# Kernel tuning notes

Hardware: AMD Instinct MI355X
Metric: run time of the kernel (lower is better)

## Reference

```python
import jax, jax.numpy as jnp
import numpy as np

B, S, D = 8, 3840, 384
G, H, E = 30, 48, 8          # groups, heads, head_dim (D == H*E)
SL = S // G                   # local window length = 128


def setup_inputs() -> dict:
    key = jax.random.key(0)
    ks = jax.random.split(key, 6)
    std = 0.05  # matches nn.init.normal_(std=0.05)
    return {
        "inputs": jax.random.normal(ks[0], (B, S, D), jnp.float32),
        "conquer": jax.random.normal(ks[1], (B, 1, D), jnp.float32),
        "mask_local": jnp.zeros((B, G, SL, SL), jnp.bool_),
        "mask_conquer": jnp.zeros((B, G, SL), jnp.bool_),
        "W_Query": jax.random.normal(ks[2], (D, D), jnp.float32) * std,
        "W_Key": jax.random.normal(ks[3], (D, D), jnp.float32) * std,
        "W_Value": jax.random.normal(ks[4], (D, D), jnp.float32) * std,
        "ln_gamma": jnp.ones((D,), jnp.float32),
        "ln_beta": jnp.zeros((D,), jnp.float32),
    }


def _layer_norm(x, gamma, beta, eps=1e-5):
    mu = jnp.mean(x, axis=-1, keepdims=True)
    var = jnp.mean(jnp.square(x - mu), axis=-1, keepdims=True)
    return (x - mu) * jax.lax.rsqrt(var + eps) * gamma + beta


def reference(inputs, conquer, mask_local, mask_conquer, W_Query, W_Key, W_Value, ln_gamma, ln_beta):
    b, s, d = inputs.shape
    N = b * G  # number of (batch, shot) groups
    x = inputs.reshape(N, SL, d)                                   # [N, SL, D]
    cq_in = jnp.broadcast_to(conquer, (b, G, d)).reshape(N, 1, d)   # [N, 1, D]
    ml = mask_local.reshape(N, SL, SL)
    mc = mask_conquer.reshape(N, SL)

    # per-head projections: [N, SL, H, E]
    q = jnp.einsum('nsd,de->nse', x, W_Query).reshape(N, SL, H, E)
    k = jnp.einsum('nsd,de->nse', x, W_Key).reshape(N, SL, H, E)
    v = jnp.einsum('nsd,de->nse', x, W_Value).reshape(N, SL, H, E)
    qc = jnp.einsum('nqd,de->nqe', cq_in, W_Query).reshape(N, 1, H, E)

    # grouped local attention (no 1/sqrt(E) scaling in the original)
    scores = jnp.einsum('nshe,nthe->nhst', q, k)                    # [N, H, SL, SL]
    scores = jnp.where(ml[:, None, :, :], -jnp.inf, scores)
    probs = jax.nn.softmax(scores, axis=-1)
    res = jnp.einsum('nhst,nthe->nshe', probs, v).reshape(N, SL, d)  # heads concat last
    res = jax.nn.relu(res)
    res = _layer_norm(res, ln_gamma, ln_beta)

    # conquer-token cross attention
    cscores = jnp.einsum('nqhe,nthe->nhqt', qc, k)[:, :, 0, :]       # [N, H, SL]
    cscores = jnp.where(mc[:, None, :], -jnp.inf, cscores)
    cprobs = jax.nn.softmax(cscores, axis=-1)
    cres = jnp.einsum('nht,nthe->nhe', cprobs, v).reshape(N, d)
    cres = jax.nn.relu(cres)  # use_relu=True

    return res.reshape(b, s, d), cres.reshape(b, G, d)
```

## Files before the change

### kernel.cpp

```cpp
#include <hip/hip_runtime.h>
#include <hip/hip_bf16.h>

#define B_   8
#define S_   3840
#define D_   384
#define G_   30
#define H_   48
#define E_   8
#define SL_  128
#define N_   (B_*G_)
#define M_   (N_*SL_)
#define NH_  (N_*H_)
#define VPAD 136

typedef __attribute__((ext_vector_type(8))) short bfrag;
typedef __attribute__((ext_vector_type(4))) float ffrag;
typedef __attribute__((ext_vector_type(16))) float f16v;

static __device__ __forceinline__ float bits2f(unsigned int u) {
    union { unsigned int i; float f; } x; x.i = u; return x.f;
}
static __device__ __forceinline__ unsigned short f2bf(float f) {
    union { float f; unsigned int i; } x; x.f = f;
    unsigned int r = x.i + 0x7fffu + ((x.i >> 16) & 1u);
    return (unsigned short)(r >> 16);
}
static __device__ __forceinline__ float bf2f(unsigned short u) {
    return bits2f(((unsigned int)u) << 16);
}
static __device__ __forceinline__ void unpack8(const unsigned short* p, float* o) {
    const uint4 raw = *reinterpret_cast<const uint4*>(p);
    o[0] = bits2f(raw.x << 16); o[1] = bits2f(raw.x & 0xffff0000u);
    o[2] = bits2f(raw.y << 16); o[3] = bits2f(raw.y & 0xffff0000u);
    o[4] = bits2f(raw.z << 16); o[5] = bits2f(raw.z & 0xffff0000u);
    o[6] = bits2f(raw.w << 16); o[7] = bits2f(raw.w & 0xffff0000u);
}

__global__ __launch_bounds__(256) void prep_kernel(
    const float* __restrict__ X, const float* __restrict__ Wq,
    const float* __restrict__ Wk, const float* __restrict__ Wv,
    const float* __restrict__ conquer,
    unsigned short* __restrict__ X2, unsigned short* __restrict__ W2t,
    float* __restrict__ qc)
{
    const int id = blockIdx.x;
    const int t  = threadIdx.x;
    if (id < 2880) {
        const int n = id / 12, ks = id % 12;
        const float* Xb = X + (size_t)n * 128 * 384;
#pragma unroll
        for (int p = 0; p < 4; ++p) {
            const int s = p * 256 + t;
            const int r = s >> 3;
            const int c = (s & 7) ^ (r & 7);
            const float4 xv = *reinterpret_cast<const float4*>(
                Xb + (size_t)r * 384 + ks * 32 + c * 4);
            uint4 pk;
            pk.x = 0x10001u * (unsigned int)f2bf(xv.x);
            pk.y = 0x10001u * (unsigned int)f2bf(xv.y);
            pk.z = 0x10001u * (unsigned int)f2bf(xv.z);
            pk.w = 0x10001u * (unsigned int)f2bf(xv.w);
            *reinterpret_cast<uint4*>(X2 + (size_t)id * 8192 + s * 8) = pk;
        }
    } else if (id < 3096) {
        const int id2 = id - 2880;
        const int nt = id2 / 12, ks = id2 % 12;
#pragma unroll
        for (int p = 0; p < 2; ++p) {
            const int s = p * 256 + t;
            const int r = s >> 3;
            const int c = (s & 7) ^ (r & 7);
            const int gn = nt * 64 + r;
            const int mat = gn / 384;
            const int wcol = gn - mat * 384;
            const float* W = (mat == 0) ? Wq : (mat == 1) ? Wk : Wv;
            const int k0 = ks * 32 + c * 4;
            unsigned int pk[4];
#pragma unroll
            for (int cc = 0; cc < 4; ++cc) {
                const float wv = W[(size_t)(k0 + cc) * 384 + wcol];
                const unsigned short hi = f2bf(wv);
                const unsigned short lo = f2bf(wv - bf2f(hi));
                pk[cc] = (unsigned int)hi | ((unsigned int)lo << 16);
            }
            uint4 out; out.x = pk[0]; out.y = pk[1]; out.z = pk[2]; out.w = pk[3];
            *reinterpret_cast<uint4*>(W2t + (size_t)id2 * 4096 + s * 8) = out;
        }
    } else {
        const int b = id - 3096;
#pragma unroll
        for (int p = 0; p < 2; ++p) {
            const int d = p * 256 + t;
            if (d < 384) {
                float acc = 0.f;
                for (int i = 0; i < 384; i++)
                    acc += conquer[b * 384 + i] * Wq[i * 384 + d];
                qc[b * 384 + d] = acc;
            }
        }
    }
}

__global__ void __launch_bounds__(256)
__attribute__((amdgpu_waves_per_eu(2, 3)))
fused_kernel(const unsigned short* __restrict__ X2,
             const unsigned short* __restrict__ W2t,
             const float* __restrict__ qcp, float* __restrict__ out0,
             float* __restrict__ out1)
{
    __shared__ unsigned short LDS[25088];
    unsigned short* Als = LDS;
    unsigned short* Bls = LDS + 8192;
    unsigned short* Qls = LDS;
    unsigned short* Kls = LDS + 8192;
    unsigned short* Vls = LDS + 16384;

    const int t    = threadIdx.x;
    const int lane = t & 63;
    const int w    = t >> 6;
    const int wm   = w >> 1, wn = w & 1;
    const int bid  = blockIdx.x;
    const int slot = bid >> 3;
    const int n    = (bid & 7) * 30 + slot / 6;
    const int cg   = slot % 6;
    const int q    = lane >> 4, r16 = lane & 15, sw = r16 & 7;
    const int l5   = lane >> 5, s31 = lane & 31;

    const unsigned short* X2n = X2 + (size_t)n * 12 * 8192;

    ffrag accQ[4][2], accK[4][2], accV[4][2];
#pragma unroll
    for (int i = 0; i < 4; ++i)
#pragma unroll
        for (int j = 0; j < 2; ++j) {
            accQ[i][j] = (ffrag)0.f; accK[i][j] = (ffrag)0.f; accV[i][j] = (ffrag)0.f;
        }

#pragma unroll 1
    for (int ks = 0; ks < 12; ++ks) {
        __syncthreads();
        {
            const unsigned short* as = X2n + (size_t)ks * 8192 + w * 2048 + lane * 8;
#pragma unroll
            for (int j2 = 0; j2 < 4; ++j2)
                __builtin_amdgcn_global_load_lds(
                    (const __attribute__((address_space(1))) void*)(as + j2 * 512),
                    (__attribute__((address_space(3))) void*)(Als + w * 2048 + j2 * 512),
                    16, 0, 0);
#pragma unroll
            for (int j2 = 0; j2 < 6; ++j2) {
                const int idx = w * 6 + j2;
                const int cls = idx >> 3;
                const int off = (idx & 7) * 512;
                const unsigned short* bs =
                    W2t + ((size_t)((cls * 6 + cg) * 12 + ks)) * 4096 + off + lane * 8;
                __builtin_amdgcn_global_load_lds(
                    (const __attribute__((address_space(1))) void*)bs,
                    (__attribute__((address_space(3))) void*)(Bls + idx * 512),
                    16, 0, 0);
            }
        }
        __syncthreads();

#pragma unroll
        for (int kk = 0; kk < 2; ++kk) {
            const int ca = (kk * 4 + q) ^ sw;
            bfrag av[4];
#pragma unroll
            for (int i = 0; i < 4; ++i)
                av[i] = *reinterpret_cast<const bfrag*>(
                    Als + ((wm * 64 + i * 16 + r16) * 8 + ca) * 8);
#pragma unroll
            for (int j = 0; j < 2; ++j) {
                const int ro = ((wn * 32 + j * 16 + r16) * 8 + ca) * 8;
                const bfrag bq_ = *reinterpret_cast<const bfrag*>(Bls + ro);
                const bfrag bk_ = *reinterpret_cast<const bfrag*>(Bls + 4096 + ro);
                const bfrag bv_ = *reinterpret_cast<const bfrag*>(Bls + 8192 + ro);
#pragma unroll
                for (int i = 0; i < 4; ++i) {
                    accQ[i][j] = __builtin_amdgcn_mfma_f32_16x16x32_bf16(bq_, av[i], accQ[i][j], 0, 0, 0);
                    accK[i][j] = __builtin_amdgcn_mfma_f32_16x16x32_bf16(bk_, av[i], accK[i][j], 0, 0, 0);
                    accV[i][j] = __builtin_amdgcn_mfma_f32_16x16x32_bf16(av[i], bv_, accV[i][j], 0, 0, 0);
                }
            }
        }
    }

    __syncthreads();

#pragma unroll
    for (int j = 0; j < 2; ++j) {
        const int wcol = wn * 32 + j * 16 + q * 4;
        const int hl = wcol >> 3;
        const int e0 = wcol & 7;
#pragma unroll
        for (int i = 0; i < 4; ++i) {
            const int s = wm * 64 + i * 16 + r16;
            uint2 pq;
            pq.x = (unsigned int)f2bf(accQ[i][j][0]) | ((unsigned int)f2bf(accQ[i][j][1]) << 16);
            pq.y = (unsigned int)f2bf(accQ[i][j][2]) | ((unsigned int)f2bf(accQ[i][j][3]) << 16);
            *reinterpret_cast<uint2*>(&Qls[hl * 1024 + s * 8 + e0]) = pq;
            uint2 pk;
            pk.x = (unsigned int)f2bf(accK[i][j][0]) | ((unsigned int)f2bf(accK[i][j][1]) << 16);
            pk.y = (unsigned int)f2bf(accK[i][j][2]) | ((unsigned int)f2bf(accK[i][j][3]) << 16);
            *reinterpret_cast<uint2*>(&Kls[hl * 1024 + s * 8 + e0]) = pk;
        }
    }
#pragma unroll
    for (int j = 0; j < 2; ++j) {
        const int wcol = wn * 32 + j * 16 + r16;
        const int hl = wcol >> 3, e = wcol & 7;
#pragma unroll
        for (int i = 0; i < 4; ++i) {
            const int s0 = wm * 64 + i * 16 + q * 4;
            uint2 pv;
            pv.x = (unsigned int)f2bf(accV[i][j][0]) | ((unsigned int)f2bf(accV[i][j][1]) << 16);
            pv.y = (unsigned int)f2bf(accV[i][j][2]) | ((unsigned int)f2bf(accV[i][j][3]) << 16);
            *reinterpret_cast<uint2*>(&Vls[hl * (VPAD * 8) + e * VPAD + s0]) = pv;
        }
    }

    __syncthreads();

#pragma unroll 1
    for (int hh = 0; hh < 2; ++hh) {
        const int hl = w * 2 + hh;
        const int hg = cg * 8 + hl;

        bfrag ak[4];
#pragma unroll
        for (int tt = 0; tt < 4; ++tt) {
#pragma unroll
            for (int r = 0; r < 8; ++r) ak[tt][r] = 0;
        }
        if (l5 == 0) {
            const unsigned short* kp = Kls + hl * 1024 + s31 * 8;
#pragma unroll
            for (int tt = 0; tt < 4; ++tt)
                ak[tt] = *reinterpret_cast<const bfrag*>(kp + tt * 256);
        }

        bfrag av2[8];
#pragma unroll
        for (int c8 = 0; c8 < 8; ++c8) {
#pragma unroll
            for (int r = 0; r < 8; ++r) av2[c8][r] = 0;
        }
        if (s31 < 8) {
            const unsigned short* vp = Vls + hl * (VPAD * 8) + s31 * VPAD + l5 * 8;
#pragma unroll
            for (int c8 = 0; c8 < 8; ++c8)
                av2[c8] = *reinterpret_cast<const bfrag*>(vp + c8 * 16);
        }

#pragma unroll 1
        for (int ss = 0; ss < 4; ++ss) {
            const bfrag bq = *reinterpret_cast<const bfrag*>(
                &Qls[hl * 1024 + (ss * 32 + s31) * 8]);
            f16v dt = (f16v)0.f;
            float lacc = 0.f;
#pragma unroll
            for (int tt = 0; tt < 4; ++tt) {
                f16v sc = __builtin_amdgcn_mfma_f32_32x32x16_bf16(ak[tt], bq, (f16v)0.f, 0, 0, 0);
                float ev[16];
                float sum = 0.f;
#pragma unroll
                for (int r = 0; r < 16; ++r) { ev[r] = __expf(sc[r]); sum += ev[r]; }
                lacc += sum + __shfl_xor(sum, 32);

                unsigned int p[8], y[8];
#pragma unroll
                for (int i2 = 0; i2 < 8; ++i2)
                    p[i2] = (unsigned int)f2bf(ev[2 * i2]) | ((unsigned int)f2bf(ev[2 * i2 + 1]) << 16);
#pragma unroll
                for (int i2 = 0; i2 < 8; ++i2)
                    y[i2] = (unsigned int)__shfl_xor((int)p[i2], 32);

                uint4 u0, u1;
                u0.x = l5 ? y[2] : p[0];  u0.y = l5 ? y[3] : p[1];
                u0.z = l5 ? p[2] : y[0];  u0.w = l5 ? p[3] : y[1];
                u1.x = l5 ? y[6] : p[4];  u1.y = l5 ? y[7] : p[5];
                u1.z = l5 ? p[6] : y[4];  u1.w = l5 ? p[7] : y[5];

                dt = __builtin_amdgcn_mfma_f32_32x32x16_bf16(
                    av2[2 * tt], *reinterpret_cast<const bfrag*>(&u0), dt, 0, 0, 0);
                dt = __builtin_amdgcn_mfma_f32_32x32x16_bf16(
                    av2[2 * tt + 1], *reinterpret_cast<const bfrag*>(&u1), dt, 0, 0, 0);
            }
            const float inv = 1.f / lacc;
            float4 o = make_float4(dt[0] * inv, dt[1] * inv, dt[2] * inv, dt[3] * inv);
            float* dst = out0 + (size_t)(n * SL_ + ss * 32 + s31) * D_ + hg * E_ + l5 * 4;
            *reinterpret_cast<float4*>(dst) = o;
        }
    }

    const int b = n / G_;
#pragma unroll 1
    for (int hh = 0; hh < 2; ++hh) {
        const int hl = w * 2 + hh;
        const int hg = cg * 8 + hl;

        float qv[8];
        const float* qp = qcp + b * D_ + hg * E_;
#pragma unroll
        for (int e = 0; e < 8; ++e) qv[e] = qp[e];

        float k0[8], k1[8], v0[8], v1[8];
        unpack8(&Kls[hl * 1024 + lane * 8], k0);
        unpack8(&Kls[hl * 1024 + (lane + 64) * 8], k1);
#pragma unroll
        for (int e = 0; e < 8; ++e) {
            v0[e] = bf2f(Vls[hl * (VPAD * 8) + e * VPAD + lane]);
            v1[e] = bf2f(Vls[hl * (VPAD * 8) + e * VPAD + 64 + lane]);
        }

        float s0 = 0.f, s1 = 0.f;
#pragma unroll
        for (int e = 0; e < 8; ++e) { s0 += qv[e] * k0[e]; s1 += qv[e] * k1[e]; }

        float mx = fmaxf(s0, s1);
#pragma unroll
        for (int off = 32; off; off >>= 1) mx = fmaxf(mx, __shfl_xor(mx, off));

        const float p0 = __expf(s0 - mx), p1 = __expf(s1 - mx);
        float l = p0 + p1;
        float o[8];
#pragma unroll
        for (int e = 0; e < 8; ++e) o[e] = p0 * v0[e] + p1 * v1[e];
#pragma unroll
        for (int off = 32; off; off >>= 1) {
            l += __shfl_xor(l, off);
#pragma unroll
            for (int e = 0; e < 8; ++e) o[e] += __shfl_xor(o[e], off);
        }
        if (lane == 0) {
            const float inv = 1.f / l;
            float* dst = out1 + (size_t)n * D_ + hg * E_;
#pragma unroll
            for (int e = 0; e < 8; ++e)
                dst[e] = fmaxf(o[e] * inv, 0.f);
        }
    }
}

__global__ __launch_bounds__(256) void ln_kernel(
    float* __restrict__ out0, const float* __restrict__ gamma,
    const float* __restrict__ beta)
{
    const int lane = threadIdx.x & 63;
    const int w    = threadIdx.x >> 6;
    const int row  = blockIdx.x * 4 + w;
    float* p = out0 + (size_t)row * D_;

    float x[6];
#pragma unroll
    for (int i = 0; i < 6; i++)
        x[i] = fmaxf(p[lane + i * 64], 0.f);

    float s = 0.f, s2 = 0.f;
#pragma unroll
    for (int i = 0; i < 6; i++) { s += x[i]; s2 += x[i] * x[i]; }
#pragma unroll
    for (int off = 32; off; off >>= 1) {
        s  += __shfl_xor(s, off);
        s2 += __shfl_xor(s2, off);
    }
    const float mu   = s * (1.f / 384.f);
    const float var  = s2 * (1.f / 384.f) - mu * mu;
    const float rstd = rsqrtf(var + 1e-5f);
#pragma unroll
    for (int i = 0; i < 6; i++) {
        const int d = lane + i * 64;
        p[d] = (x[i] - mu) * rstd * gamma[d] + beta[d];
    }
}

extern "C" void kernel_launch(void* const* d_in, const int* in_sizes, int n_in,
                              void* d_out, int out_size, void* d_ws, size_t ws_size,
                              hipStream_t stream)
{
    const float* X       = (const float*)d_in[0];
    const float* conquer = (const float*)d_in[1];
    const float* Wq      = (const float*)d_in[4];
    const float* Wk      = (const float*)d_in[5];
    const float* Wv      = (const float*)d_in[6];
    const float* gamma   = (const float*)d_in[7];
    const float* beta    = (const float*)d_in[8];

    float* out0 = (float*)d_out;
    float* out1 = out0 + (size_t)M_ * D_;

    unsigned short* X2  = (unsigned short*)d_ws;
    unsigned short* W2t = X2 + (size_t)240 * 12 * 8192;
    float* qcp = (float*)(W2t + (size_t)18 * 12 * 4096);

    prep_kernel<<<dim3(3104), 256, 0, stream>>>(X, Wq, Wk, Wv, conquer, X2, W2t, qcp);
    fused_kernel<<<dim3(1440), 256, 0, stream>>>(X2, W2t, qcp, out0, out1);
    ln_kernel<<<dim3(M_ / 4), 256, 0, stream>>>(out0, gamma, beta);
}
```

Baseline: 268.6 us.

## Double-buffer weight tiles in LDS, load X fragments directly, and truncate probabilities

The projection loop now double-buffers the weight tiles in LDS, issuing the DMA for the next k-step while computing on the current one. The X tile no longer goes through LDS: each wave reads its A fragments straight from global memory, so the prep kernel drops the XOR swizzle. The occupancy hint is raised from 2-3 to 3-4 waves per EU. Softmax probabilities are packed to bf16 by truncation with a byte permute instead of round-to-nearest, which saves ALU work at a small accuracy cost. Direct global fragment loads could add latency, and the higher occupancy target could force register spills.

```diff
diff --git a/kernel.cpp b/kernel.cpp
--- a/kernel.cpp
+++ b/kernel.cpp
@@ -20,9 +20,12 @@
 static __device__ __forceinline__ float bits2f(unsigned int u) {
     union { unsigned int i; float f; } x; x.i = u; return x.f;
 }
+static __device__ __forceinline__ unsigned int f2u(float f) {
+    union { float f; unsigned int i; } x; x.f = f; return x.i;
+}
 static __device__ __forceinline__ unsigned short f2bf(float f) {
-    union { float f; unsigned int i; } x; x.f = f;
-    unsigned int r = x.i + 0x7fffu + ((x.i >> 16) & 1u);
+    unsigned int i = f2u(f);
+    unsigned int r = i + 0x7fffu + ((i >> 16) & 1u);
     return (unsigned short)(r >> 16);
 }
 static __device__ __forceinline__ float bf2f(unsigned short u) {
@@ -52,7 +55,7 @@
         for (int p = 0; p < 4; ++p) {
             const int s = p * 256 + t;
             const int r = s >> 3;
-            const int c = (s & 7) ^ (r & 7);
+            const int c = s & 7;
             const float4 xv = *reinterpret_cast<const float4*>(
                 Xb + (size_t)r * 384 + ks * 32 + c * 4);
             uint4 pk;
@@ -102,18 +105,18 @@
 }
 
 __global__ void __launch_bounds__(256)
-__attribute__((amdgpu_waves_per_eu(2, 3)))
+__attribute__((amdgpu_waves_per_eu(3, 4)))
 fused_kernel(const unsigned short* __restrict__ X2,
              const unsigned short* __restrict__ W2t,
              const float* __restrict__ qcp, float* __restrict__ out0,
              float* __restrict__ out1)
 {
     __shared__ unsigned short LDS[25088];
-    unsigned short* Als = LDS;
-    unsigned short* Bls = LDS + 8192;
-    unsigned short* Qls = LDS;
-    unsigned short* Kls = LDS + 8192;
-    unsigned short* Vls = LDS + 16384;
+    unsigned short* Bst0 = LDS;
+    unsigned short* Bst1 = LDS + 12288;
+    unsigned short* Qls  = LDS;
+    unsigned short* Kls  = LDS + 8192;
+    unsigned short* Vls  = LDS + 16384;
 
     const int t    = threadIdx.x;
     const int lane = t & 63;
@@ -136,57 +139,57 @@
             accQ[i][j] = (ffrag)0.f; accK[i][j] = (ffrag)0.f; accV[i][j] = (ffrag)0.f;
         }
 
+    auto dmaB = [&](int ks, unsigned short* dst) {
+#pragma unroll
+        for (int j2 = 0; j2 < 6; ++j2) {
+            const int idx = w * 6 + j2;
+            const int cls = idx >> 3;
+            const int off = (idx & 7) * 512;
+            const unsigned short* bs =
+                W2t + ((size_t)((cls * 6 + cg) * 12 + ks)) * 4096 + off + lane * 8;
+            __builtin_amdgcn_global_load_lds(
+                (const __attribute__((address_space(1))) void*)bs,
+                (__attribute__((address_space(3))) void*)(dst + idx * 512),
+                16, 0, 0);
+        }
+    };
+
+    dmaB(0, Bst0);
+    __syncthreads();
+
 #pragma unroll 1
     for (int ks = 0; ks < 12; ++ks) {
-        __syncthreads();
-        {
-            const unsigned short* as = X2n + (size_t)ks * 8192 + w * 2048 + lane * 8;
-#pragma unroll
-            for (int j2 = 0; j2 < 4; ++j2)
-                __builtin_amdgcn_global_load_lds(
-                    (const __attribute__((address_space(1))) void*)(as + j2 * 512),
-                    (__attribute__((address_space(3))) void*)(Als + w * 2048 + j2 * 512),
-                    16, 0, 0);
-#pragma unroll
-            for (int j2 = 0; j2 < 6; ++j2) {
-                const int idx = w * 6 + j2;
-                const int cls = idx >> 3;
-                const int off = (idx & 7) * 512;
-                const unsigned short* bs =
-                    W2t + ((size_t)((cls * 6 + cg) * 12 + ks)) * 4096 + off + lane * 8;
-                __builtin_amdgcn_global_load_lds(
-                    (const __attribute__((address_space(1))) void*)bs,
-                    (__attribute__((address_space(3))) void*)(Bls + idx * 512),
-                    16, 0, 0);
-            }
-        }
-        __syncthreads();
+        unsigned short* Bcur = (ks & 1) ? Bst1 : Bst0;
+        if (ks < 11) dmaB(ks + 1, (ks & 1) ? Bst0 : Bst1);
+
+        bfrag av[4][2];
+#pragma unroll
+        for (int i = 0; i < 4; ++i)
+#pragma unroll
+            for (int kk = 0; kk < 2; ++kk)
+                av[i][kk] = *reinterpret_cast<const bfrag*>(
+                    X2n + (size_t)ks * 8192 +
+                    ((wm * 64 + i * 16 + r16) * 8 + kk * 4 + q) * 8);
 
 #pragma unroll
         for (int kk = 0; kk < 2; ++kk) {
             const int ca = (kk * 4 + q) ^ sw;
-            bfrag av[4];
-#pragma unroll
-            for (int i = 0; i < 4; ++i)
-                av[i] = *reinterpret_cast<const bfrag*>(
-                    Als + ((wm * 64 + i * 16 + r16) * 8 + ca) * 8);
 #pragma unroll
             for (int j = 0; j < 2; ++j) {
                 const int ro = ((wn * 32 + j * 16 + r16) * 8 + ca) * 8;
-                const bfrag bq_ = *reinterpret_cast<const bfrag*>(Bls + ro);
-                const bfrag bk_ = *reinterpret_cast<const bfrag*>(Bls + 4096 + ro);
-                const bfrag bv_ = *reinterpret_cast<const bfrag*>(Bls + 8192 + ro);
+                const bfrag bq_ = *reinterpret_cast<const bfrag*>(Bcur + ro);
+                const bfrag bk_ = *reinterpret_cast<const bfrag*>(Bcur + 4096 + ro);
+                const bfrag bv_ = *reinterpret_cast<const bfrag*>(Bcur + 8192 + ro);
 #pragma unroll
                 for (int i = 0; i < 4; ++i) {
-                    accQ[i][j] = __builtin_amdgcn_mfma_f32_16x16x32_bf16(bq_, av[i], accQ[i][j], 0, 0, 0);
-                    accK[i][j] = __builtin_amdgcn_mfma_f32_16x16x32_bf16(bk_, av[i], accK[i][j], 0, 0, 0);
-                    accV[i][j] = __builtin_amdgcn_mfma_f32_16x16x32_bf16(av[i], bv_, accV[i][j], 0, 0, 0);
+                    accQ[i][j] = __builtin_amdgcn_mfma_f32_16x16x32_bf16(bq_, av[i][kk], accQ[i][j], 0, 0, 0);
+                    accK[i][j] = __builtin_amdgcn_mfma_f32_16x16x32_bf16(bk_, av[i][kk], accK[i][j], 0, 0, 0);
+                    accV[i][j] = __builtin_amdgcn_mfma_f32_16x16x32_bf16(av[i][kk], bv_, accV[i][j], 0, 0, 0);
                 }
             }
         }
-    }
-
-    __syncthreads();
+        __syncthreads();
+    }
 
 #pragma unroll
     for (int j = 0; j < 2; ++j) {
@@ -271,7 +274,8 @@
                 unsigned int p[8], y[8];
 #pragma unroll
                 for (int i2 = 0; i2 < 8; ++i2)
-                    p[i2] = (unsigned int)f2bf(ev[2 * i2]) | ((unsigned int)f2bf(ev[2 * i2 + 1]) << 16);
+                    p[i2] = __builtin_amdgcn_perm(
+                        f2u(ev[2 * i2 + 1]), f2u(ev[2 * i2]), 0x07060302u);
 #pragma unroll
                 for (int i2 = 0; i2 < 8; ++i2)
                     y[i2] = (unsigned int)__shfl_xor((int)p[i2], 32);
```

After: 273.8 us. Within noise of the previous version (+2.0%).
